# Kernel optimization log

Hardware: AMD Instinct MI355X
Metric: run time of the kernel (lower is better)

Reference implementation:

```python
import jax, jax.numpy as jnp
import numpy as np

N = 2000
E = 20000
C = 16
B = 128
N_IN = 200   # first N_IN nodes are input nodes
N_OUT = 200  # last N_OUT nodes are output nodes
EPS = 1e-5


def setup_inputs() -> dict:
    key = jax.random.key(0)
    ks = jax.random.split(key, 8)
    x = jax.random.normal(ks[0], (B, N), dtype=jnp.float32)
    edge_index = jax.random.randint(ks[1], (2, E), 0, N, dtype=jnp.int32)
    input_node_mask = jnp.arange(N) < N_IN
    output_node_mask = jnp.arange(N) >= (N - N_OUT)
    func_mask = ~(input_node_mask | output_node_mask)
    # sparse-linear parameters (structured forms of W1/W2/W3)
    w1 = jax.random.normal(ks[2], (E, C), dtype=jnp.float32) * (1.0 / np.sqrt(C))
    b1 = jnp.zeros((N, C), dtype=jnp.float32)
    w2 = jax.random.normal(ks[3], (N, C, C), dtype=jnp.float32) * (1.0 / np.sqrt(C))
    b2 = jnp.zeros((N, C), dtype=jnp.float32)
    w3 = jax.random.normal(ks[4], (E, C), dtype=jnp.float32) * 1.0  # d=1 init scale
    b3 = jnp.zeros((E,), dtype=jnp.float32)
    g1 = jnp.ones((N * C,), dtype=jnp.float32)
    be1 = jnp.zeros((N * C,), dtype=jnp.float32)
    g2 = jnp.ones((N * C,), dtype=jnp.float32)
    be2 = jnp.zeros((N * C,), dtype=jnp.float32)
    return {"x": x, "w1": w1, "b1": b1, "w2": w2, "b2": b2, "w3": w3, "b3": b3,
            "g1": g1, "be1": be1, "g2": g2, "be2": be2,
            "edge_index": edge_index, "func_mask": func_mask,
            "output_node_mask": output_node_mask, "layers": 4}


def _batchnorm(h, g, b):
    # training-mode BatchNorm1d: batch mean and biased variance over axis 0
    m = h.mean(axis=0)
    v = h.var(axis=0)
    return (h - m) * jax.lax.rsqrt(v + EPS) * g + b


def reference(x, w1, b1, w2, b2, w3, b3, g1, be1, g2, be2,
              edge_index, func_mask, output_node_mask, layers):
    src, dst = edge_index[0], edge_index[1]
    Bsz, Nn = x.shape
    Ee, Cc = w1.shape
    fm = func_mask.astype(x.dtype)
    w2m = w2 * fm[:, None, None]          # W2 blocks exist only at function nodes
    w3m = w3 * fm[src][:, None]           # W3 rows exist only for edges with src in function nodes

    x0 = x[:, src]                        # node2edge: (B, E)
    xe = x0
    for _ in range(layers):
        # lin1: scatter edge values into dst node hidden channels
        contrib = xe.T[:, :, None] * w1[:, None, :]                    # (E, B, C)
        h = jax.ops.segment_sum(contrib, dst, num_segments=Nn)         # (N, B, C)
        h = jnp.transpose(h, (1, 0, 2)) + b1                           # (B, N, C)
        h = _batchnorm(h.reshape(Bsz, Nn * Cc), g1, be1)
        h = jax.nn.elu(h).reshape(Bsz, Nn, Cc)
        # lin2: block-diagonal C x C mix per (function) node
        h = jnp.einsum('bnc,ncd->bnd', h, w2m) + b2
        h = _batchnorm(h.reshape(Bsz, Nn * Cc), g2, be2)
        h = jax.nn.elu(h).reshape(Bsz, Nn, Cc)
        # lin3: gather src hidden, per-edge dot back to edge space
        xe = jnp.einsum('bec,ec->be', h[:, src], w3m) + b3             # (B, E)
        xe = xe + x0
    # edge2node: scatter-sum edge values to dst nodes, keep output nodes
    nodes = jax.ops.segment_sum(xe.T, dst, num_segments=Nn)            # (N, B)
    return nodes.T * output_node_mask.astype(x.dtype)
```

## Files before the change

kernel.cpp:

```cpp
#include <hip/hip_runtime.h>
#include <math.h>

#define BB 128
#define NN 2000
#define EE 20000
#define CC 16
#define FUNC_LO 200
#define FUNC_HI 1800
#define OUT_LO 1800
#define OUTN 200
#define NFUNC 1600
#define EPSV 1e-5f
#define SS 40
#define HP 129

__global__ void k_assign(const int* __restrict__ ei, int* __restrict__ degIn,
                         int* __restrict__ degOut, int* __restrict__ posIn,
                         int* __restrict__ posOut) {
    int e = blockIdx.x * 256 + threadIdx.x;
    if (e < EE) {
        int s = ei[e], d = ei[EE + e];
        int p = atomicAdd(&degIn[d], 1);
        int q = atomicAdd(&degOut[s], 1);
        posIn[e]  = d * SS + p;
        posOut[e] = s * SS + q;
    }
}

__global__ void k_presort(const float* __restrict__ x, const int* __restrict__ ei,
                          const int* __restrict__ posIn, const int* __restrict__ posOut,
                          const float* __restrict__ w1, const float* __restrict__ w3,
                          const float* __restrict__ b3,
                          float* __restrict__ xT, float* __restrict__ w1s,
                          float* __restrict__ w3s, float* __restrict__ b3s,
                          int* __restrict__ inoff, int* __restrict__ wout,
                          int* __restrict__ dstn) {
    int t = blockIdx.x * 256 + threadIdx.x;
    if (t < EE * CC) {
        int e = t >> 4, c = t & 15;
        w1s[posIn[e]  * CC + c] = w1[t];
        w3s[posOut[e] * CC + c] = w3[t];
    }
    if (t < EE) {
        int pi = posIn[t], po = posOut[t];
        inoff[pi] = ei[t] * BB;
        wout[po]  = pi * BB;
        dstn[po]  = ei[EE + t];
        b3s[po]   = b3[t];
    }
    if (t < NN * BB) {
        int b = t / NN, n = t - b * NN;
        xT[n * BB + b] = x[t];
    }
}

__global__ __launch_bounds__(128) void k_fill(
    const int* __restrict__ ei, const int* __restrict__ posIn,
    const float* __restrict__ b3, const float* __restrict__ xT,
    float* __restrict__ xeA, float* __restrict__ xeB, float* __restrict__ outT)
{
    int e = blockIdx.x;
    int s = ei[e];
    if (s >= FUNC_LO && s < FUNC_HI) return;
    int d = ei[EE + e];
    int b = threadIdx.x;
    float val = b3[e] + xT[s * BB + b];
    if (d >= FUNC_LO && d < FUNC_HI) {
        int ro = posIn[e] * BB;
        xeA[ro + b] = val;
        xeB[ro + b] = val;
    } else if (d >= OUT_LO) {
        atomicAdd(&outT[(d - OUT_LO) * BB + b], val);
    }
}

__device__ __forceinline__ void bn_elu(float (&t)[CC],
                                       const float* __restrict__ g,
                                       const float* __restrict__ be,
                                       float* tile, float* part_s, float* part_ss,
                                       float* sc, float* sh, int b) {
    #pragma unroll
    for (int c = 0; c < CC; c++) tile[c * HP + b] = t[c];
    __syncthreads();
    {
        int c = b & 15, grp = b >> 4;
        float s = 0.f, ss = 0.f;
        #pragma unroll
        for (int i = 0; i < 16; i++) {
            float v = tile[c * HP + grp * 16 + i];
            s += v; ss += v * v;
        }
        part_s[grp * 16 + c] = s;
        part_ss[grp * 16 + c] = ss;
    }
    __syncthreads();
    if (b < CC) {
        float S = 0.f, SSm = 0.f;
        #pragma unroll
        for (int g8 = 0; g8 < 8; g8++) { S += part_s[g8 * 16 + b]; SSm += part_ss[g8 * 16 + b]; }
        float mean = S * (1.0f / BB);
        float var = SSm * (1.0f / BB) - mean * mean;
        float scale = rsqrtf(var + EPSV) * g[b];
        sc[b] = scale;
        sh[b] = be[b] - mean * scale;
    }
    __syncthreads();
    #pragma unroll
    for (int c = 0; c < CC; c++) {
        float u = t[c] * sc[c] + sh[c];
        t[c] = (u > 0.0f) ? u : (__expf(u) - 1.0f);
    }
}

__global__ __launch_bounds__(128) void k_layer(
    const float* __restrict__ xe_in, const int* __restrict__ inoff,
    const float* __restrict__ xT,
    const float* __restrict__ w1s, const float* __restrict__ w2,
    const float* __restrict__ w3s, const float* __restrict__ b3s,
    const int* __restrict__ wout, const int* __restrict__ dstn,
    const float* __restrict__ g1, const float* __restrict__ be1,
    const float* __restrict__ g2, const float* __restrict__ be2,
    const int* __restrict__ degIn, const int* __restrict__ degOut,
    float* __restrict__ xe_out, float* __restrict__ outT, int lastFlag)
{
    const int b = threadIdx.x;
    const int n = FUNC_LO + blockIdx.x;
    const int base = n * SS;

    __shared__ float tile[CC * HP];
    __shared__ float part_s[128], part_ss[128];
    __shared__ float sc[CC], sh[CC];

    int dIn = degIn[n];
    int dOut = degOut[n];
    float x0r = xT[n * BB + b];

    float a[CC];
    #pragma unroll
    for (int c = 0; c < CC; c++) a[c] = 0.0f;

    for (int k0 = 0; k0 < dIn; k0 += 8) {
        float v[8];
        #pragma unroll
        for (int j = 0; j < 8; j++) {
            v[j] = 0.0f;
            if (k0 + j < dIn) {
                int ro = inoff ? inoff[base + k0 + j] : (base + k0 + j) * BB;
                v[j] = xe_in[ro + b];
            }
        }
        #pragma unroll
        for (int j = 0; j < 8; j++) {
            if (k0 + j < dIn) {
                const float* wr = &w1s[(size_t)(base + k0 + j) * CC];
                #pragma unroll
                for (int c = 0; c < CC; c++) a[c] += v[j] * wr[c];
            }
        }
    }

    bn_elu(a, g1 + n * CC, be1 + n * CC, tile, part_s, part_ss, sc, sh, b);

    float h2[CC];
    #pragma unroll
    for (int d = 0; d < CC; d++) h2[d] = 0.0f;
    const float* w2n = w2 + n * (CC * CC);
    #pragma unroll
    for (int c = 0; c < CC; c++) {
        float av = a[c];
        #pragma unroll
        for (int d = 0; d < CC; d++) h2[d] += av * w2n[c * CC + d];
    }

    bn_elu(h2, g2 + n * CC, be2 + n * CC, tile, part_s, part_ss, sc, sh, b);

    for (int q0 = 0; q0 < dOut; q0 += 4) {
        #pragma unroll
        for (int j = 0; j < 4; j++) {
            int q = q0 + j;
            if (q >= dOut) break;
            int sl = base + q;
            int dn = dstn[sl];
            bool live = lastFlag ? (dn >= OUT_LO) : (dn >= FUNC_LO && dn < FUNC_HI);
            if (!live) continue;
            const float* wr = &w3s[(size_t)sl * CC];
            float val = b3s[sl] + x0r;
            #pragma unroll
            for (int d = 0; d < CC; d++) val += h2[d] * wr[d];
            if (lastFlag) atomicAdd(&outT[(dn - OUT_LO) * BB + b], val);
            else          xe_out[wout[sl] + b] = val;
        }
    }
}

__global__ void k_finalize(const float* __restrict__ outT, float* __restrict__ out) {
    int idx = blockIdx.x * 256 + threadIdx.x;
    if (idx < BB * NN) {
        int b = idx / NN;
        int n = idx - b * NN;
        out[idx] = (n >= OUT_LO) ? outT[(n - OUT_LO) * BB + b] : 0.0f;
    }
}

extern "C" void kernel_launch(void* const* d_in, const int* in_sizes, int n_in,
                              void* d_out, int out_size, void* d_ws, size_t ws_size,
                              hipStream_t stream) {
    const float* x   = (const float*)d_in[0];
    const float* w1  = (const float*)d_in[1];
    const float* w2  = (const float*)d_in[3];
    const float* w3  = (const float*)d_in[5];
    const float* b3  = (const float*)d_in[6];
    const float* g1  = (const float*)d_in[7];
    const float* be1 = (const float*)d_in[8];
    const float* g2  = (const float*)d_in[9];
    const float* be2 = (const float*)d_in[10];
    const int* ei    = (const int*)d_in[11];
    float* out = (float*)d_out;

    char* ws = (char*)d_ws;
    float* xT   = (float*)ws;  ws += (size_t)NN * BB * 4;
    float* xeA  = (float*)ws;  ws += (size_t)NN * SS * BB * 4;
    float* xeB  = (float*)ws;  ws += (size_t)NN * SS * BB * 4;
    float* w1s  = (float*)ws;  ws += (size_t)NN * SS * CC * 4;
    float* w3s  = (float*)ws;  ws += (size_t)NN * SS * CC * 4;
    float* b3s  = (float*)ws;  ws += (size_t)NN * SS * 4;
    float* outT = (float*)ws;  ws += (size_t)OUTN * BB * 4;
    int* degIn  = (int*)ws;    ws += (size_t)NN * 4;
    int* degOut = (int*)ws;    ws += (size_t)NN * 4;
    int* posIn  = (int*)ws;    ws += (size_t)EE * 4;
    int* posOut = (int*)ws;    ws += (size_t)EE * 4;
    int* inoff  = (int*)ws;    ws += (size_t)NN * SS * 4;
    int* wout   = (int*)ws;    ws += (size_t)NN * SS * 4;
    int* dstn   = (int*)ws;    ws += (size_t)NN * SS * 4;

    hipMemsetAsync(degIn, 0, 2 * NN * sizeof(int), stream);
    hipMemsetAsync(outT, 0, (size_t)OUTN * BB * 4, stream);
    k_assign<<<(EE + 255) / 256, 256, 0, stream>>>(ei, degIn, degOut, posIn, posOut);
    k_presort<<<(EE * CC + 255) / 256, 256, 0, stream>>>(x, ei, posIn, posOut, w1, w3, b3,
                                                         xT, w1s, w3s, b3s,
                                                         inoff, wout, dstn);
    k_fill<<<EE, 128, 0, stream>>>(ei, posIn, b3, xT, xeA, xeB, outT);

    k_layer<<<NFUNC, 128, 0, stream>>>(xT,  inoff,   xT, w1s, w2, w3s, b3s, wout, dstn,
                                       g1, be1, g2, be2, degIn, degOut, xeA, outT, 0);
    k_layer<<<NFUNC, 128, 0, stream>>>(xeA, nullptr, xT, w1s, w2, w3s, b3s, wout, dstn,
                                       g1, be1, g2, be2, degIn, degOut, xeB, outT, 0);
    k_layer<<<NFUNC, 128, 0, stream>>>(xeB, nullptr, xT, w1s, w2, w3s, b3s, wout, dstn,
                                       g1, be1, g2, be2, degIn, degOut, xeA, outT, 0);
    k_layer<<<NFUNC, 128, 0, stream>>>(xeA, nullptr, xT, w1s, w2, w3s, b3s, wout, dstn,
                                       g1, be1, g2, be2, degIn, degOut, xeB, outT, 1);

    k_finalize<<<(NN * BB + 255) / 256, 256, 0, stream>>>(outT, out);
}
```

Baseline: 165.2 us.

## Fuse prep kernels, fold fill into first layer, drop finalize pass

```diff
diff --git a/kernel.cpp b/kernel.cpp
--- a/kernel.cpp
+++ b/kernel.cpp
@@ -8,69 +8,46 @@
 #define FUNC_LO 200
 #define FUNC_HI 1800
 #define OUT_LO 1800
-#define OUTN 200
 #define NFUNC 1600
 #define EPSV 1e-5f
 #define SS 40
 #define HP 129
-
-__global__ void k_assign(const int* __restrict__ ei, int* __restrict__ degIn,
-                         int* __restrict__ degOut, int* __restrict__ posIn,
-                         int* __restrict__ posOut) {
-    int e = blockIdx.x * 256 + threadIdx.x;
-    if (e < EE) {
-        int s = ei[e], d = ei[EE + e];
+#define NPB 2
+#define NBLK (NFUNC / NPB)
+#define TPB (128 * NPB)
+
+__global__ __launch_bounds__(256) void k_prep(
+    const float* __restrict__ x, const int* __restrict__ ei,
+    const float* __restrict__ w1, const float* __restrict__ w3,
+    const float* __restrict__ b3,
+    int* __restrict__ degIn, int* __restrict__ degOut,
+    int* __restrict__ posIn,
+    float* __restrict__ xT, float* __restrict__ w1s, float* __restrict__ w3s,
+    float* __restrict__ b3s, int* __restrict__ inoff, int* __restrict__ wout,
+    int* __restrict__ dstn, float* __restrict__ out)
+{
+    int t = blockIdx.x * 256 + threadIdx.x;
+    if (t < EE) {
+        int s = ei[t], d = ei[EE + t];
         int p = atomicAdd(&degIn[d], 1);
         int q = atomicAdd(&degOut[s], 1);
-        posIn[e]  = d * SS + p;
-        posOut[e] = s * SS + q;
-    }
-}
-
-__global__ void k_presort(const float* __restrict__ x, const int* __restrict__ ei,
-                          const int* __restrict__ posIn, const int* __restrict__ posOut,
-                          const float* __restrict__ w1, const float* __restrict__ w3,
-                          const float* __restrict__ b3,
-                          float* __restrict__ xT, float* __restrict__ w1s,
-                          float* __restrict__ w3s, float* __restrict__ b3s,
-                          int* __restrict__ inoff, int* __restrict__ wout,
-                          int* __restrict__ dstn) {
-    int t = blockIdx.x * 256 + threadIdx.x;
-    if (t < EE * CC) {
-        int e = t >> 4, c = t & 15;
-        w1s[posIn[e]  * CC + c] = w1[t];
-        w3s[posOut[e] * CC + c] = w3[t];
-    }
-    if (t < EE) {
-        int pi = posIn[t], po = posOut[t];
-        inoff[pi] = ei[t] * BB;
+        int pi = d * SS + p, po = s * SS + q;
+        posIn[t] = pi;
+        inoff[pi] = s * BB;
         wout[po]  = pi * BB;
-        dstn[po]  = ei[EE + t];
+        dstn[po]  = d;
         b3s[po]   = b3[t];
+        const float4* w1r = (const float4*)(w1 + (size_t)t * CC);
+        float4*       w1d = (float4*)(w1s + (size_t)pi * CC);
+        const float4* w3r = (const float4*)(w3 + (size_t)t * CC);
+        float4*       w3d = (float4*)(w3s + (size_t)po * CC);
+        #pragma unroll
+        for (int i = 0; i < 4; i++) { w1d[i] = w1r[i]; w3d[i] = w3r[i]; }
     }
     if (t < NN * BB) {
         int b = t / NN, n = t - b * NN;
         xT[n * BB + b] = x[t];
-    }
-}
-
-__global__ __launch_bounds__(128) void k_fill(
-    const int* __restrict__ ei, const int* __restrict__ posIn,
-    const float* __restrict__ b3, const float* __restrict__ xT,
-    float* __restrict__ xeA, float* __restrict__ xeB, float* __restrict__ outT)
-{
-    int e = blockIdx.x;
-    int s = ei[e];
-    if (s >= FUNC_LO && s < FUNC_HI) return;
-    int d = ei[EE + e];
-    int b = threadIdx.x;
-    float val = b3[e] + xT[s * BB + b];
-    if (d >= FUNC_LO && d < FUNC_HI) {
-        int ro = posIn[e] * BB;
-        xeA[ro + b] = val;
-        xeB[ro + b] = val;
-    } else if (d >= OUT_LO) {
-        atomicAdd(&outT[(d - OUT_LO) * BB + b], val);
+        out[t] = 0.0f;
     }
 }
 
@@ -112,7 +89,7 @@
     }
 }
 
-__global__ __launch_bounds__(128) void k_layer(
+__device__ __forceinline__ void layer_body(
     const float* __restrict__ xe_in, const int* __restrict__ inoff,
     const float* __restrict__ xT,
     const float* __restrict__ w1s, const float* __restrict__ w2,
@@ -121,16 +98,11 @@
     const float* __restrict__ g1, const float* __restrict__ be1,
     const float* __restrict__ g2, const float* __restrict__ be2,
     const int* __restrict__ degIn, const int* __restrict__ degOut,
-    float* __restrict__ xe_out, float* __restrict__ outT, int lastFlag)
-{
-    const int b = threadIdx.x;
-    const int n = FUNC_LO + blockIdx.x;
+    float* __restrict__ xe_out, float* __restrict__ out, int lastFlag,
+    float* tile, float* part_s, float* part_ss, float* sc, float* sh,
+    int n, int b)
+{
     const int base = n * SS;
-
-    __shared__ float tile[CC * HP];
-    __shared__ float part_s[128], part_ss[128];
-    __shared__ float sc[CC], sh[CC];
-
     int dIn = degIn[n];
     int dOut = degOut[n];
     float x0r = xT[n * BB + b];
@@ -187,19 +159,62 @@
             float val = b3s[sl] + x0r;
             #pragma unroll
             for (int d = 0; d < CC; d++) val += h2[d] * wr[d];
-            if (lastFlag) atomicAdd(&outT[(dn - OUT_LO) * BB + b], val);
+            if (lastFlag) atomicAdd(&out[(size_t)b * NN + dn], val);
             else          xe_out[wout[sl] + b] = val;
         }
     }
 }
 
-__global__ void k_finalize(const float* __restrict__ outT, float* __restrict__ out) {
-    int idx = blockIdx.x * 256 + threadIdx.x;
-    if (idx < BB * NN) {
-        int b = idx / NN;
-        int n = idx - b * NN;
-        out[idx] = (n >= OUT_LO) ? outT[(n - OUT_LO) * BB + b] : 0.0f;
-    }
+__device__ __forceinline__ void fill_body(const int* __restrict__ ei,
+    const int* __restrict__ posIn, const float* __restrict__ b3,
+    const float* __restrict__ xT, float* __restrict__ xeA, float* __restrict__ xeB,
+    float* __restrict__ out, int gtid, int gsize)
+{
+    for (int t = gtid; t < EE * BB; t += gsize) {
+        int e = t >> 7, bb = t & 127;
+        int s = ei[e];
+        if (s >= FUNC_LO && s < FUNC_HI) continue;
+        int d = ei[EE + e];
+        float val = b3[e] + xT[s * BB + bb];
+        if (d >= FUNC_LO && d < FUNC_HI) {
+            int ro = posIn[e] * BB;
+            xeA[ro + bb] = val;
+            xeB[ro + bb] = val;
+        } else if (d >= OUT_LO) {
+            atomicAdd(&out[(size_t)bb * NN + d], val);
+        }
+    }
+}
+
+__global__ __launch_bounds__(TPB) void k_stage(
+    const int* __restrict__ ei, const int* __restrict__ posIn,
+    const float* __restrict__ b3,
+    const float* __restrict__ xe_in, const int* __restrict__ inoff,
+    const float* __restrict__ xT,
+    const float* __restrict__ w1s, const float* __restrict__ w2,
+    const float* __restrict__ w3s, const float* __restrict__ b3s,
+    const int* __restrict__ wout, const int* __restrict__ dstn,
+    const float* __restrict__ g1, const float* __restrict__ be1,
+    const float* __restrict__ g2, const float* __restrict__ be2,
+    const int* __restrict__ degIn, const int* __restrict__ degOut,
+    float* __restrict__ xeA, float* __restrict__ xeB,
+    float* __restrict__ xe_out, float* __restrict__ out, int lastFlag, int doFill)
+{
+    __shared__ float tile[NPB][CC * HP];
+    __shared__ float part_s[NPB][128], part_ss[NPB][128];
+    __shared__ float sc[NPB][CC], sh[NPB][CC];
+
+    const int tid = threadIdx.x;
+    const int half = tid >> 7;
+    const int b = tid & 127;
+    const int n = FUNC_LO + blockIdx.x * NPB + half;
+
+    if (doFill)
+        fill_body(ei, posIn, b3, xT, xeA, xeB, out, blockIdx.x * TPB + tid, NBLK * TPB);
+
+    layer_body(xe_in, inoff, xT, w1s, w2, w3s, b3s, wout, dstn, g1, be1, g2, be2,
+               degIn, degOut, xe_out, out, lastFlag,
+               tile[half], part_s[half], part_ss[half], sc[half], sh[half], n, b);
 }
 
 extern "C" void kernel_launch(void* const* d_in, const int* in_sizes, int n_in,
@@ -224,31 +239,29 @@
     float* w1s  = (float*)ws;  ws += (size_t)NN * SS * CC * 4;
     float* w3s  = (float*)ws;  ws += (size_t)NN * SS * CC * 4;
     float* b3s  = (float*)ws;  ws += (size_t)NN * SS * 4;
-    float* outT = (float*)ws;  ws += (size_t)OUTN * BB * 4;
     int* degIn  = (int*)ws;    ws += (size_t)NN * 4;
     int* degOut = (int*)ws;    ws += (size_t)NN * 4;
     int* posIn  = (int*)ws;    ws += (size_t)EE * 4;
-    int* posOut = (int*)ws;    ws += (size_t)EE * 4;
     int* inoff  = (int*)ws;    ws += (size_t)NN * SS * 4;
     int* wout   = (int*)ws;    ws += (size_t)NN * SS * 4;
     int* dstn   = (int*)ws;    ws += (size_t)NN * SS * 4;
 
     hipMemsetAsync(degIn, 0, 2 * NN * sizeof(int), stream);
-    hipMemsetAsync(outT, 0, (size_t)OUTN * BB * 4, stream);
-    k_assign<<<(EE + 255) / 256, 256, 0, stream>>>(ei, degIn, degOut, posIn, posOut);
-    k_presort<<<(EE * CC + 255) / 256, 256, 0, stream>>>(x, ei, posIn, posOut, w1, w3, b3,
-                                                         xT, w1s, w3s, b3s,
-                                                         inoff, wout, dstn);
-    k_fill<<<EE, 128, 0, stream>>>(ei, posIn, b3, xT, xeA, xeB, outT);
-
-    k_layer<<<NFUNC, 128, 0, stream>>>(xT,  inoff,   xT, w1s, w2, w3s, b3s, wout, dstn,
-                                       g1, be1, g2, be2, degIn, degOut, xeA, outT, 0);
-    k_layer<<<NFUNC, 128, 0, stream>>>(xeA, nullptr, xT, w1s, w2, w3s, b3s, wout, dstn,
-                                       g1, be1, g2, be2, degIn, degOut, xeB, outT, 0);
-    k_layer<<<NFUNC, 128, 0, stream>>>(xeB, nullptr, xT, w1s, w2, w3s, b3s, wout, dstn,
-                                       g1, be1, g2, be2, degIn, degOut, xeA, outT, 0);
-    k_layer<<<NFUNC, 128, 0, stream>>>(xeA, nullptr, xT, w1s, w2, w3s, b3s, wout, dstn,
-                                       g1, be1, g2, be2, degIn, degOut, xeB, outT, 1);
-
-    k_finalize<<<(NN * BB + 255) / 256, 256, 0, stream>>>(outT, out);
-}
+    k_prep<<<(NN * BB) / 256, 256, 0, stream>>>(x, ei, w1, w3, b3, degIn, degOut,
+                                                posIn, xT, w1s, w3s, b3s,
+                                                inoff, wout, dstn, out);
+
+    const int* nullp = nullptr;
+    k_stage<<<NBLK, TPB, 0, stream>>>(ei, posIn, b3, xT, inoff, xT, w1s, w2, w3s, b3s,
+                                      wout, dstn, g1, be1, g2, be2, degIn, degOut,
+                                      xeA, xeB, xeA, out, 0, 1);
+    k_stage<<<NBLK, TPB, 0, stream>>>(ei, posIn, b3, xeA, nullp, xT, w1s, w2, w3s, b3s,
+                                      wout, dstn, g1, be1, g2, be2, degIn, degOut,
+                                      xeA, xeB, xeB, out, 0, 0);
+    k_stage<<<NBLK, TPB, 0, stream>>>(ei, posIn, b3, xeB, nullp, xT, w1s, w2, w3s, b3s,
+                                      wout, dstn, g1, be1, g2, be2, degIn, degOut,
+                                      xeA, xeB, xeA, out, 0, 0);
+    k_stage<<<NBLK, TPB, 0, stream>>>(ei, posIn, b3, xeA, nullp, xT, w1s, w2, w3s, b3s,
+                                      wout, dstn, g1, be1, g2, be2, degIn, degOut,
+                                      xeA, xeB, xeB, out, 1, 0);
+}
```

After: 223.4 us. 1.35x slower.
